# Performance work log

Hardware: AMD Instinct MI355X
Metric: run time of the kernel (lower is better)

Reference implementation:

```python
import math
import jax, jax.numpy as jnp
import numpy as np

B, S, D_MODEL = 4, 1024, 512
D_BAR, C_ONSET, N_HEADS = 256, 32, 8
T_ONSET, POOL = 8192, 8


def setup_inputs() -> dict:
    key = jax.random.key(0)
    ks = jax.random.split(key, 16)
    p = lambda i, shape: jax.random.normal(ks[i], shape, dtype=jnp.float32) * 0.05
    return {
        "token_embs": jax.random.normal(ks[0], (B, S, D_MODEL), dtype=jnp.float32),
        "onset_1d": jax.random.uniform(ks[1], (B, T_ONSET, C_ONSET), dtype=jnp.float32),
        "bar_mask": jax.random.bernoulli(ks[2], 0.0625, (B, S)),  # ~1 bar / 16 tokens
        "Wih_note": p(3, (3 * D_BAR, D_MODEL)),
        "Whh_note": p(4, (3 * D_BAR, D_BAR)),
        "bih_note": p(5, (3 * D_BAR,)),
        "bhh_note": p(6, (3 * D_BAR,)),
        "Wih_bar": p(7, (3 * D_BAR, D_BAR)),
        "Whh_bar": p(8, (3 * D_BAR, D_BAR)),
        "bih_bar": p(9, (3 * D_BAR,)),
        "bhh_bar": p(10, (3 * D_BAR,)),
        "Wq": p(11, (D_BAR, D_BAR)),
        "bq": p(12, (D_BAR,)),
        "Wk": p(13, (D_BAR, C_ONSET)),
        "bk": p(14, (D_BAR,)),
        "pos_bias_scale": jnp.float32(2.5),
    }


def _gru_cell(x, h, Wih, Whh, bih, bhh):
    # torch nn.GRU cell, gate order (r, z, n)
    gi = x @ Wih.T + bih
    gh = h @ Whh.T + bhh
    ir, iz, inn = jnp.split(gi, 3, axis=-1)
    hr, hz, hn = jnp.split(gh, 3, axis=-1)
    r = jax.nn.sigmoid(ir + hr)
    z = jax.nn.sigmoid(iz + hz)
    n = jnp.tanh(inn + r * hn)
    return (1.0 - z) * n + z * h


def _sinusoidal_pe(T, C, dtype):
    half = C // 2
    pos = jnp.arange(T, dtype=dtype)
    div = jnp.exp(jnp.arange(half, dtype=dtype) * (-math.log(10000.0) / half))
    ang = pos[:, None] * div[None, :]  # [T, half]
    # interleave sin/cos -> [T, C] (C even)
    return jnp.stack([jnp.sin(ang), jnp.cos(ang)], axis=-1).reshape(T, C)


def _forward(token_embs, onset_1d, bar_mask, Wih_note, Whh_note, bih_note, bhh_note,
             Wih_bar, Whh_bar, bih_bar, bhh_bar, Wq, bq, Wk, bk, pos_bias_scale):
    Bc, Sc, _ = token_embs.shape
    d_bar = Whh_bar.shape[1]
    H = N_HEADS
    dh = d_bar // H
    dtype = token_embs.dtype

    # --- audio keys: avg_pool1d(k=8,s=8) + sinusoidal PE + projection ---
    T = onset_1d.shape[1]
    pooled = onset_1d.reshape(Bc, T // POOL, POOL, onset_1d.shape[2]).mean(axis=2)  # [B,T_oct,C]
    T_oct = pooled.shape[1]
    pe = _sinusoidal_pe(T_oct, pooled.shape[2], dtype)
    K = (pooled + pe[None]) @ Wk.T + bk  # [B,T_oct,d_bar]

    # --- fused note-GRU / bar-GRU scan over sequence positions ---
    # Segment semantics: bar tokens are excluded from note-GRU segments; at a
    # <bar> position the note hidden (= bar summary; zero for empty segments)
    # feeds one bar-GRU step, then the note hidden resets to zero.
    def step(carry, xs):
        h_note, g_bar = carry
        x, m = xs  # x: [B,D], m: [B] bool
        h_next = _gru_cell(x, h_note, Wih_note, Whh_note, bih_note, bhh_note)
        g_next = _gru_cell(h_note, g_bar, Wih_bar, Whh_bar, bih_bar, bhh_bar)
        m_ = m[:, None]
        g_out = jnp.where(m_, g_next, g_bar)
        h_out = jnp.where(m_, jnp.zeros_like(h_next), h_next)
        return (h_out, g_out), g_out

    zeros = jnp.zeros((Bc, d_bar), dtype=dtype)
    (_, g_end), g_seq = jax.lax.scan(
        step, (zeros, zeros),
        (token_embs.transpose(1, 0, 2), bar_mask.T))
    h_bar_carried = g_seq.transpose(1, 0, 2)  # [B,S,d_bar]: h_bar after most recent bar <= s
    h_bar_final = g_end[None]                 # [1,B,d_bar]

    # --- cross-attention com_t (computed densely, masked to <bar> positions) ---
    Q = (h_bar_carried @ Wq.T + bq).reshape(Bc, Sc, H, dh)
    K4 = K.reshape(Bc, T_oct, H, dh)
    scores = jnp.einsum('bshd,bthd->bsht', Q, K4) / math.sqrt(dh)
    time_pos = jnp.linspace(0.0, 1.0, T_oct, dtype=dtype)
    scores = scores - pos_bias_scale * time_pos  # broadcast pos bias over t
    attn = jax.nn.softmax(scores, axis=-1)
    com = jnp.sum(attn.mean(axis=2) * time_pos, axis=-1)  # [B,S]
    com_t_all = jnp.where(bar_mask, com, 0.0)[..., None]  # [B,S,1]

    return com_t_all, h_bar_final, h_bar_carried


def reference(token_embs, onset_1d, bar_mask, Wih_note, Whh_note, bih_note, bhh_note,
              Wih_bar, Whh_bar, bih_bar, bhh_bar, Wq, bq, Wk, bk, pos_bias_scale):
    return _forward(token_embs, onset_1d, bar_mask, Wih_note, Whh_note, bih_note, bhh_note,
                    Wih_bar, Whh_bar, bih_bar, bhh_bar, Wq, bq, Wk, bk, pos_bias_scale)
```

## Files before the change

### kernel.cpp

```cpp
#include <hip/hip_runtime.h>
#include <hip/hip_bf16.h>
#include <math.h>

#define NB 4
#define SEQ 1024
#define DM 512
#define DB 256
#define G3 768
#define CO 32
#define TONS 8192
#define POOLN 8
#define TOCT 1024
#define NH 8
#define DHD 32

#define RKT 5
#define LKT 3

#define OFF_GI     0u
#define OFF_GIBAR  3145728u
#define OFF_HEND   6291456u
#define OFF_GALL   7340032u
#define OFF_KMAT   8388608u
#define OFF_WFN    9437184u
#define OFF_WFB    9633792u
#define OFF_INT_BYTES 39321600u

#define OUT_FINAL 4096
#define OUT_CARR  5120

typedef __attribute__((ext_vector_type(8))) short short8v;
typedef __attribute__((ext_vector_type(4))) float f32x4;

__device__ __forceinline__ unsigned int bf16rne(float f) {
    unsigned int u = __float_as_uint(f);
    return (u + 0x7fffu + ((u >> 16) & 1u)) >> 16;
}

__global__ __launch_bounds__(256) void k_scan(const unsigned char* __restrict__ mraw,
        int* __restrict__ pos, int* __restrict__ lastk, int* __restrict__ nmask,
        int* __restrict__ sS, int* __restrict__ sLen, int* __restrict__ sC,
        int* __restrict__ nseg) {
    __shared__ int rnz[8];
    __shared__ int gt1;
    __shared__ int mode;
    __shared__ int snm[NB];
    int tid = threadIdx.x;
    if (tid < 8) rnz[tid] = 0;
    if (tid == 0) gt1 = 0;
    __syncthreads();
    for (int i = tid; i < NB * SEQ; i += 256) {
        unsigned char v = mraw[i];
        if (v) {
            rnz[i & 7] = 1;
            if (v > 1) gt1 = 1;
        }
    }
    __syncthreads();
    if (tid == 0) {
        bool lowhalf = rnz[0] | rnz[1] | rnz[4] | rnz[5];
        bool hihalf  = rnz[2] | rnz[3] | rnz[6] | rnz[7];
        int m;
        if (hihalf && !lowhalf) {
            m = (rnz[2] | rnz[3]) ? 3 : 4;
        } else if (gt1) {
            m = 5;
        } else if (rnz[1] | rnz[3] | rnz[5] | rnz[7]) {
            m = 0;
        } else if (rnz[4]) {
            m = 1;
        } else if (rnz[0]) {
            m = 2;
        } else {
            m = 0;
        }
        mode = m;
    }
    __syncthreads();
    if (tid < NB) {
        int b = tid;
        int cnt = 0;
        for (int t = 0; t < SEQ; ++t) {
            int idx = b * SEQ + t;
            int mv;
            switch (mode) {
                case 0:  mv = mraw[idx] != 0; break;
                case 1:  mv = ((const int*)mraw)[idx] != 0; break;
                case 2:  mv = ((const long long*)mraw)[idx] != 0LL; break;
                case 3:  mv = ((const float*)mraw)[idx] != 0.f; break;
                case 4:  mv = ((const double*)mraw)[idx] != 0.0; break;
                default: mv = ((const unsigned short*)mraw)[idx] != 0; break;
            }
            if (mv) { pos[b * SEQ + cnt] = t; ++cnt; }
            lastk[idx] = cnt - 1;
        }
        nmask[b] = cnt;
        snm[b] = cnt;
    }
    __syncthreads();
    if (tid < NB) {
        int b = tid;
        int base = 0;
        for (int x = 0; x < b; ++x) base += snm[x];
        int cnt = snm[b];
        for (int k = 0; k < cnt; ++k) {
            int e = pos[b * SEQ + k];
            int s = (k == 0) ? 0 : (pos[b * SEQ + k - 1] + 1);
            sS[base + k]   = b * SEQ + s;
            sLen[base + k] = e - s;
            sC[base + k]   = b * SEQ + k;
        }
    }
    __syncthreads();
    if (tid == 0) {
        int t = 0;
        for (int x = 0; x < NB; ++x) t += snm[x];
        *nseg = t;
    }
}

__global__ __launch_bounds__(256) void k_wfrag(const float* __restrict__ W, uint4* __restrict__ out) {
    int idx = blockIdx.x * 256 + threadIdx.x;
    if (idx >= 48 * 8 * 64) return;
    int lane = idx & 63;
    int TK = idx >> 6;
    int T = TK >> 3, Kt = TK & 7;
    int row = 16 * T + (lane & 15);
    int kb = 32 * Kt + (lane >> 4) * 8;
    const float* wr = W + (size_t)row * DB + kb;
    uint4 u;
    u.x = bf16rne(wr[0]) | (bf16rne(wr[1]) << 16);
    u.y = bf16rne(wr[2]) | (bf16rne(wr[3]) << 16);
    u.z = bf16rne(wr[4]) | (bf16rne(wr[5]) << 16);
    u.w = bf16rne(wr[6]) | (bf16rne(wr[7]) << 16);
    out[idx] = u;
}

__global__ __launch_bounds__(256) void k_gemm_nt(int M, int N, int K,
        const float* __restrict__ A, const float* __restrict__ Bm,
        const float* __restrict__ bias, float* __restrict__ C) {
    __shared__ __align__(16) float As2[32][68];
    __shared__ __align__(16) float Bs2[32][68];
    int bm = blockIdx.y * 64, bn = blockIdx.x * 64;
    int tid = threadIdx.x;
    int tx = tid & 15, ty = tid >> 4;
    float acc[4][4] = {};
    for (int k0 = 0; k0 < K; k0 += 32) {
        for (int i = tid; i < 64 * 32; i += 256) {
            int r = i >> 5, c = i & 31;
            As2[c][r] = A[(size_t)(bm + r) * K + k0 + c];
            Bs2[c][r] = Bm[(size_t)(bn + r) * K + k0 + c];
        }
        __syncthreads();
#pragma unroll
        for (int kk = 0; kk < 32; ++kk) {
            float4 av = *reinterpret_cast<const float4*>(&As2[kk][ty * 4]);
            float4 bv = *reinterpret_cast<const float4*>(&Bs2[kk][tx * 4]);
            float a[4] = {av.x, av.y, av.z, av.w};
            float b[4] = {bv.x, bv.y, bv.z, bv.w};
#pragma unroll
            for (int i = 0; i < 4; ++i)
#pragma unroll
                for (int j = 0; j < 4; ++j) acc[i][j] += a[i] * b[j];
        }
        __syncthreads();
    }
#pragma unroll
    for (int i = 0; i < 4; ++i)
#pragma unroll
        for (int j = 0; j < 4; ++j)
            C[(size_t)(bm + ty * 4 + i) * N + bn + tx * 4 + j] = acc[i][j] + bias[bn + tx * 4 + j];
}

__global__ __launch_bounds__(64) void k_keys(const float* __restrict__ onset,
        const float* __restrict__ Wk, const float* __restrict__ bk, float* __restrict__ Kmat) {
    int bt = blockIdx.x;
    int b = bt >> 10, t = bt & 1023;
    __shared__ float xin[CO];
    int tid = threadIdx.x;
    if (tid < CO) {
        float s = 0.f;
        const float* base = onset + ((size_t)b * TONS + (size_t)t * POOLN) * CO + tid;
#pragma unroll
        for (int p = 0; p < POOLN; ++p) s += base[p * CO];
        s *= (1.f / POOLN);
        int j = tid >> 1;
        float dv = expf(-logf(10000.f) * (float)j / 16.f);
        float ang = (float)t * dv;
        s += (tid & 1) ? cosf(ang) : sinf(ang);
        xin[tid] = s;
    }
    __syncthreads();
    for (int n = tid; n < DB; n += 64) {
        float acc = bk[n];
        const float* wr = Wk + (size_t)n * CO;
#pragma unroll
        for (int c = 0; c < CO; ++c) acc += xin[c] * wr[c];
        Kmat[(size_t)bt * DB + n] = acc;
    }
}

template<int MODE>
__global__ __launch_bounds__(512, 1) void k_gru(
        const uint4* __restrict__ wf, const float* __restrict__ bhh,
        const float* __restrict__ gx_src,
        const int* __restrict__ sS, const int* __restrict__ sLen,
        const int* __restrict__ sC, const int* __restrict__ nseg_p,
        const int* __restrict__ nmask, float* __restrict__ outp) {
    int bg = blockIdx.x;
    int nseg = (MODE == 0) ? *nseg_p : NB;
    if (16 * bg >= nseg) return;
    int tid = threadIdx.x;
    int w = tid >> 6;
    int lane = tid & 63;
    int lhi = lane >> 4, c = lane & 15;

    __shared__ __align__(16) unsigned short hfrag[8 * 64 * 8];
    __shared__ __align__(16) uint4 wlds[8 * 6 * LKT * 64];

    uint4 wreg[6][RKT];
#pragma unroll
    for (int t = 0; t < 6; ++t) {
        int T = 16 * (t >> 1) + 2 * w + (t & 1);
#pragma unroll
        for (int kt = 0; kt < RKT; ++kt)
            wreg[t][kt] = wf[(size_t)(T * 8 + kt) * 64 + lane];
#pragma unroll
        for (int kt = 0; kt < LKT; ++kt)
            wlds[((w * 6 + t) * LKT + kt) * 64 + lane] = wf[(size_t)(T * 8 + RKT + kt) * 64 + lane];
    }

    int ss_r[4], len_r[4], sc_r[4];
#pragma unroll
    for (int r = 0; r < 4; ++r) {
        int m = 4 * lhi + r;
        int gs = 16 * bg + m;
        if (MODE == 0) {
            bool v = gs < nseg;
            ss_r[r]  = v ? sS[gs] : 0;
            len_r[r] = v ? sLen[gs] : 0;
            sc_r[r]  = v ? sC[gs] : 0;
        } else {
            bool v = m < NB;
            ss_r[r]  = v ? m * SEQ : 0;
            len_r[r] = v ? nmask[m] : 0;
            sc_r[r]  = 0;
        }
    }
    int mx = 0;
    for (int q = 0; q < 16; ++q) {
        int gs = 16 * bg + q;
        int L = (MODE == 0) ? ((gs < nseg) ? sLen[gs] : 0)
                            : ((q < NB) ? nmask[q] : 0);
        mx = max(mx, L);
    }
    float bh[3][2];
#pragma unroll
    for (int g = 0; g < 3; ++g)
#pragma unroll
        for (int ii = 0; ii < 2; ++ii)
            bh[g][ii] = bhh[g * 256 + 32 * w + 16 * ii + c];
    float h[4][2] = {};

    for (int i = 0; i < mx; ++i) {
        float gx[3][2][4];
#pragma unroll
        for (int r = 0; r < 4; ++r) {
            int row = (i < len_r[r]) ? (ss_r[r] + i) : ss_r[r];
            const float* gp = gx_src + (size_t)row * G3 + 32 * w + c;
#pragma unroll
            for (int g = 0; g < 3; ++g)
#pragma unroll
                for (int ii = 0; ii < 2; ++ii)
                    gx[g][ii][r] = gp[g * 256 + 16 * ii];
        }
        f32x4 acc[6];
#pragma unroll
        for (int t = 0; t < 6; ++t) acc[t] = (f32x4){0.f, 0.f, 0.f, 0.f};
        if (i > 0) {
            const short8v* hf8 = (const short8v*)hfrag;
#pragma unroll
            for (int kt = 0; kt < 8; ++kt) {
                short8v a = hf8[kt * 64 + lane];
                if (kt < RKT) {
#pragma unroll
                    for (int t = 0; t < 6; ++t) {
                        short8v bv = __builtin_bit_cast(short8v, wreg[t][kt]);
                        acc[t] = __builtin_amdgcn_mfma_f32_16x16x32_bf16(a, bv, acc[t], 0, 0, 0);
                    }
                } else {
#pragma unroll
                    for (int t = 0; t < 6; ++t) {
                        uint4 u = wlds[((w * 6 + t) * LKT + (kt - RKT)) * 64 + lane];
                        short8v bv = __builtin_bit_cast(short8v, u);
                        acc[t] = __builtin_amdgcn_mfma_f32_16x16x32_bf16(a, bv, acc[t], 0, 0, 0);
                    }
                }
            }
        }
#pragma unroll
        for (int r = 0; r < 4; ++r) {
#pragma unroll
            for (int ii = 0; ii < 2; ++ii) {
                float rr = 1.f / (1.f + expf(-(gx[0][ii][r] + bh[0][ii] + acc[0 + ii][r])));
                float zz = 1.f / (1.f + expf(-(gx[1][ii][r] + bh[1][ii] + acc[2 + ii][r])));
                float nn = tanhf(gx[2][ii][r] + rr * (bh[2][ii] + acc[4 + ii][r]));
                float hv = (1.f - zz) * nn + zz * h[r][ii];
                bool act = i < len_r[r];
                hv = act ? hv : h[r][ii];
                h[r][ii] = hv;
                if (MODE == 1) {
                    if (lhi == 0 && act) {
                        int j = 32 * w + 16 * ii + c;
                        outp[(size_t)(ss_r[r] + i) * DB + j] = hv;
                    }
                }
            }
        }
        __syncthreads();
#pragma unroll
        for (int r = 0; r < 4; ++r)
#pragma unroll
            for (int ii = 0; ii < 2; ++ii) {
                int j = 32 * w + 16 * ii + c;
                int m = 4 * lhi + r;
                int lp = m + 16 * ((j >> 3) & 3);
                hfrag[(size_t)(w * 64 + lp) * 8 + (j & 7)] = (unsigned short)bf16rne(h[r][ii]);
            }
        __syncthreads();
    }
    if (MODE == 0) {
#pragma unroll
        for (int r = 0; r < 4; ++r) {
            int gs = 16 * bg + 4 * lhi + r;
            if (gs < nseg) {
#pragma unroll
                for (int ii = 0; ii < 2; ++ii)
                    outp[(size_t)sc_r[r] * DB + 32 * w + 16 * ii + c] = h[r][ii];
            }
        }
    }
}

__global__ __launch_bounds__(256) void k_fill(const float* __restrict__ gall,
        const int* __restrict__ lastk, const int* __restrict__ nmask,
        float* __restrict__ out) {
    int bt = blockIdx.x;
    int b = bt >> 10, t = bt & 1023;
    int tid = threadIdx.x;
    int lk = lastk[bt];
    float v = (lk >= 0) ? gall[((size_t)b * SEQ + lk) * DB + tid] : 0.f;
    out[OUT_CARR + (size_t)bt * DB + tid] = v;
    if (tid == 0) out[bt] = 0.f;
    if (t == 0) {
        int nm = nmask[b];
        float fv = (nm > 0) ? gall[((size_t)b * SEQ + nm - 1) * DB + tid] : 0.f;
        out[OUT_FINAL + b * DB + tid] = fv;
    }
}

__global__ __launch_bounds__(256) void k_attn(const float* __restrict__ gall,
        const float* __restrict__ Wq, const float* __restrict__ bq,
        const float* __restrict__ Kmat, const int* __restrict__ pos,
        const int* __restrict__ nmask, const float* __restrict__ pbs_ptr,
        float* __restrict__ out) {
    int c = blockIdx.x;
    int b = c >> 10, k = c & 1023;
    if (k >= nmask[b]) return;
    int trow = pos[b * SEQ + k];
    __shared__ float q[DB];
    __shared__ float grow[DB];
    __shared__ float sc[NH][TOCT];
    __shared__ float comh[NH];
    int tid = threadIdx.x;
    grow[tid] = gall[((size_t)b * SEQ + k) * DB + tid];
    __syncthreads();
    {
        float acc = bq[tid];
        const float* wr = Wq + (size_t)tid * DB;
#pragma unroll 4
        for (int j = 0; j < DB; ++j) acc += grow[j] * wr[j];
        q[tid] = acc;
    }
    __syncthreads();
    float pbs = *pbs_ptr;
    const float scale = 0.17677669529663687f;
    for (int t = tid; t < TOCT; t += 256) {
        const float* kr = Kmat + ((size_t)b * TOCT + t) * DB;
        float tp = (float)t * (1.f / 1023.f);
#pragma unroll
        for (int h = 0; h < NH; ++h) {
            float acc = 0.f;
#pragma unroll
            for (int d = 0; d < DHD; ++d) acc += q[h * DHD + d] * kr[h * DHD + d];
            sc[h][t] = acc * scale - pbs * tp;
        }
    }
    __syncthreads();
    int hh = tid >> 5, l = tid & 31;
    float mx = -1e30f;
    for (int t = l; t < TOCT; t += 32) mx = fmaxf(mx, sc[hh][t]);
#pragma unroll
    for (int o = 16; o > 0; o >>= 1) mx = fmaxf(mx, __shfl_xor(mx, o, 32));
    float se = 0.f, sw = 0.f;
    for (int t = l; t < TOCT; t += 32) {
        float e = expf(sc[hh][t] - mx);
        se += e;
        sw += e * ((float)t * (1.f / 1023.f));
    }
#pragma unroll
    for (int o = 16; o > 0; o >>= 1) { se += __shfl_xor(se, o, 32); sw += __shfl_xor(sw, o, 32); }
    if (l == 0) comh[hh] = sw / se;
    __syncthreads();
    if (tid == 0) {
        float cm = 0.f;
#pragma unroll
        for (int h = 0; h < NH; ++h) cm += comh[h];
        out[b * SEQ + trow] = cm * (1.f / NH);
    }
}

extern "C" void kernel_launch(void* const* d_in, const int* in_sizes, int n_in,
                              void* d_out, int out_size, void* d_ws, size_t ws_size,
                              hipStream_t stream) {
    const float* te    = (const float*)d_in[0];
    const float* onset = (const float*)d_in[1];
    const unsigned char* mask = (const unsigned char*)d_in[2];
    const float* Wih_n = (const float*)d_in[3];
    const float* Whh_n = (const float*)d_in[4];
    const float* bih_n = (const float*)d_in[5];
    const float* bhh_n = (const float*)d_in[6];
    const float* Wih_b = (const float*)d_in[7];
    const float* Whh_b = (const float*)d_in[8];
    const float* bih_b = (const float*)d_in[9];
    const float* bhh_b = (const float*)d_in[10];
    const float* Wq    = (const float*)d_in[11];
    const float* bq    = (const float*)d_in[12];
    const float* Wk    = (const float*)d_in[13];
    const float* bk    = (const float*)d_in[14];
    const float* pbs   = (const float*)d_in[15];
    float* out = (float*)d_out;

    float* ws    = (float*)d_ws;
    float* gi    = ws + OFF_GI;
    float* gibar = ws + OFF_GIBAR;
    float* hend  = ws + OFF_HEND;
    float* gall  = ws + OFF_GALL;
    float* kmat  = ws + OFF_KMAT;
    uint4* wfn   = (uint4*)(ws + OFF_WFN);
    uint4* wfb   = (uint4*)(ws + OFF_WFB);
    int* ipos    = (int*)((char*)d_ws + OFF_INT_BYTES);
    int* ilastk  = ipos + NB * SEQ;
    int* inmask  = ilastk + NB * SEQ;
    int* isS     = inmask + NB;
    int* isLen   = isS + NB * SEQ;
    int* isC     = isLen + NB * SEQ;
    int* inseg   = isC + NB * SEQ;

    k_scan<<<1, 256, 0, stream>>>(mask, ipos, ilastk, inmask, isS, isLen, isC, inseg);
    k_wfrag<<<96, 256, 0, stream>>>(Whh_n, wfn);
    k_wfrag<<<96, 256, 0, stream>>>(Whh_b, wfb);
    k_gemm_nt<<<dim3(G3 / 64, (NB * SEQ) / 64), 256, 0, stream>>>(NB * SEQ, G3, DM, te, Wih_n, bih_n, gi);
    k_keys<<<NB * TOCT, 64, 0, stream>>>(onset, Wk, bk, kmat);
    k_gru<0><<<256, 512, 0, stream>>>(wfn, bhh_n, gi, isS, isLen, isC, inseg, inmask, hend);
    k_gemm_nt<<<dim3(G3 / 64, (NB * SEQ) / 64), 256, 0, stream>>>(NB * SEQ, G3, DB, hend, Wih_b, bih_b, gibar);
    k_gru<1><<<1, 512, 0, stream>>>(wfb, bhh_b, gibar, isS, isLen, isC, inseg, inmask, gall);
    k_fill<<<NB * SEQ, 256, 0, stream>>>(gall, ilastk, inmask, out);
    k_attn<<<NB * SEQ, 256, 0, stream>>>(gall, Wq, bq, kmat, ipos, inmask, pbs, out);
}
```

Measured before the change: 1.040 ms.

## Double-buffer GRU hidden fragments, prefetch next-step gates, keep more weights in registers

```diff
diff --git a/kernel.cpp b/kernel.cpp
--- a/kernel.cpp
+++ b/kernel.cpp
@@ -14,8 +14,8 @@
 #define NH 8
 #define DHD 32
 
-#define RKT 5
-#define LKT 3
+#define RKT 6
+#define LKT 2
 
 #define OFF_GI     0u
 #define OFF_GIBAR  3145728u
@@ -215,7 +215,7 @@
     int lane = tid & 63;
     int lhi = lane >> 4, c = lane & 15;
 
-    __shared__ __align__(16) unsigned short hfrag[8 * 64 * 8];
+    __shared__ __align__(16) unsigned short hfrag[2][8 * 64 * 8];
     __shared__ __align__(16) uint4 wlds[8 * 6 * LKT * 64];
 
     uint4 wreg[6][RKT];
@@ -262,23 +262,32 @@
             bh[g][ii] = bhh[g * 256 + 32 * w + 16 * ii + c];
     float h[4][2] = {};
 
+#define LOADGX(dst, step)                                                        \
+    {                                                                            \
+        int i_ = (step);                                                         \
+        _Pragma("unroll")                                                        \
+        for (int r = 0; r < 4; ++r) {                                            \
+            int row = (i_ < len_r[r]) ? (ss_r[r] + i_) : ss_r[r];                \
+            const float* gp = gx_src + (size_t)row * G3 + 32 * w + c;            \
+            _Pragma("unroll")                                                    \
+            for (int g = 0; g < 3; ++g)                                          \
+                _Pragma("unroll")                                                \
+                for (int ii = 0; ii < 2; ++ii)                                   \
+                    dst[g][ii][r] = gp[g * 256 + 16 * ii];                       \
+        }                                                                        \
+    }
+
+    float gxa[3][2][4], gxb[3][2][4];
+    if (mx > 0) LOADGX(gxa, 0)
+    int buf = 0;
+
     for (int i = 0; i < mx; ++i) {
-        float gx[3][2][4];
-#pragma unroll
-        for (int r = 0; r < 4; ++r) {
-            int row = (i < len_r[r]) ? (ss_r[r] + i) : ss_r[r];
-            const float* gp = gx_src + (size_t)row * G3 + 32 * w + c;
-#pragma unroll
-            for (int g = 0; g < 3; ++g)
-#pragma unroll
-                for (int ii = 0; ii < 2; ++ii)
-                    gx[g][ii][r] = gp[g * 256 + 16 * ii];
-        }
+        LOADGX(gxb, i + 1)
         f32x4 acc[6];
 #pragma unroll
         for (int t = 0; t < 6; ++t) acc[t] = (f32x4){0.f, 0.f, 0.f, 0.f};
         if (i > 0) {
-            const short8v* hf8 = (const short8v*)hfrag;
+            const short8v* hf8 = (const short8v*)hfrag[buf];
 #pragma unroll
             for (int kt = 0; kt < 8; ++kt) {
                 short8v a = hf8[kt * 64 + lane];
@@ -302,9 +311,9 @@
         for (int r = 0; r < 4; ++r) {
 #pragma unroll
             for (int ii = 0; ii < 2; ++ii) {
-                float rr = 1.f / (1.f + expf(-(gx[0][ii][r] + bh[0][ii] + acc[0 + ii][r])));
-                float zz = 1.f / (1.f + expf(-(gx[1][ii][r] + bh[1][ii] + acc[2 + ii][r])));
-                float nn = tanhf(gx[2][ii][r] + rr * (bh[2][ii] + acc[4 + ii][r]));
+                float rr = 1.f / (1.f + expf(-(gxa[0][ii][r] + bh[0][ii] + acc[0 + ii][r])));
+                float zz = 1.f / (1.f + expf(-(gxa[1][ii][r] + bh[1][ii] + acc[2 + ii][r])));
+                float nn = tanhf(gxa[2][ii][r] + rr * (bh[2][ii] + acc[4 + ii][r]));
                 float hv = (1.f - zz) * nn + zz * h[r][ii];
                 bool act = i < len_r[r];
                 hv = act ? hv : h[r][ii];
@@ -317,7 +326,6 @@
                 }
             }
         }
-        __syncthreads();
 #pragma unroll
         for (int r = 0; r < 4; ++r)
 #pragma unroll
@@ -325,10 +333,20 @@
                 int j = 32 * w + 16 * ii + c;
                 int m = 4 * lhi + r;
                 int lp = m + 16 * ((j >> 3) & 3);
-                hfrag[(size_t)(w * 64 + lp) * 8 + (j & 7)] = (unsigned short)bf16rne(h[r][ii]);
+                hfrag[buf ^ 1][(size_t)(w * 64 + lp) * 8 + (j & 7)] =
+                    (unsigned short)bf16rne(h[r][ii]);
             }
         __syncthreads();
-    }
+        buf ^= 1;
+#pragma unroll
+        for (int g = 0; g < 3; ++g)
+#pragma unroll
+            for (int ii = 0; ii < 2; ++ii)
+#pragma unroll
+                for (int r = 0; r < 4; ++r)
+                    gxa[g][ii][r] = gxb[g][ii][r];
+    }
+#undef LOADGX
     if (MODE == 0) {
 #pragma unroll
         for (int r = 0; r < 4; ++r) {
```

After: 1.178 ms. +13.3%, slower.
